# Kernel tuning notes

Hardware: AMD Instinct MI355X
Metric: run time of the kernel (lower is better)

Reference implementation:

```python
import jax, jax.numpy as jnp
import numpy as np
from jax.scipy.linalg import expm

S = 64          # alphabet size (codons)
M = 8           # number of models, prod(model_shape)
N_LEAVES = 32   # leaves of the balanced binary tree
N_EDGES = 62    # nodes 0..62, every non-root node has one parent edge (edge id == child node id)
B = 1024        # batch (alignment columns)
# per-level ranges of child-node ids; node 32+j has children (2j, 2j+1), etc.
LEVELS = [(0, 32), (32, 48), (48, 56), (56, 60), (60, 62)]


def inv_stereographic_projection(p):
    # maps R^{s-1} -> unit sphere S^{s-1}
    n2 = jnp.sum(p * p, axis=-1, keepdims=True)
    return jnp.concatenate([2.0 * p / (n2 + 1.0), (n2 - 1.0) / (n2 + 1.0)], axis=-1)


def generator(R, pi):
    # R: (M, s(s-1)/2) exchangeabilities, pi: (M, s) stationary distribution
    iu, ju = np.triu_indices(S, 1)
    A = jnp.zeros((M, S, S), R.dtype).at[:, iu, ju].set(R).at[:, ju, iu].set(R)
    Q = A * pi[:, None, :]                       # Q_ij = A_ij * pi_j (off-diagonal)
    row = jnp.sum(Q, axis=-1)                    # (M, S)
    return Q - jnp.eye(S, dtype=Q.dtype) * row[:, :, None]


def felsenstein(leave_configuration, R_inv, pi_inv, lengths):
    pi = inv_stereographic_projection(pi_inv) ** 2           # (M, S), rows sum to 1
    R = jnp.exp(R_inv)                                       # positive rates
    Q = generator(R, pi)                                     # (M, S, S)
    tQ = lengths[:, None, None, None] * Q[None]              # (E, M, S, S)
    P = jax.vmap(expm)(tQ.reshape(-1, S, S)).reshape(N_EDGES, M, S, S)
    # leaf alphas: tile leaf observations over the M models -> (n_leaves, B, M, S)
    prev = jnp.broadcast_to(
        leave_configuration.transpose(1, 0, 2)[:, :, None, :],
        (N_LEAVES, leave_configuration.shape[0], M, S))
    # level-synchronous pruning: messages up each parent edge, then product of the two children
    for a, b in LEVELS:
        msg = jnp.einsum('emcd,ebmd->ebmc', P[a:b], prev)    # per-edge transition
        prev = msg[0::2] * msg[1::2]                         # combine sibling pairs
    root = prev[0]                                           # (B, M, S)
    out = jnp.einsum('bms,ms->bm', root, pi)                 # P(data | model m)
    return out.reshape(out.shape[0], M)                      # (B, *model_shape)


def setup_inputs() -> dict:
    key = jax.random.key(0)
    k1, k2, k3, k4 = jax.random.split(key, 4)
    leave_configuration = jax.random.uniform(k1, (B, N_LEAVES, S), dtype=jnp.float32)
    tree_indices = jnp.zeros((B,), dtype=jnp.int32)          # single tree (F=1)
    R_inv = jax.random.uniform(k2, (M, S * (S - 1) // 2), dtype=jnp.float32,
                               minval=-1.0, maxval=1.0)
    pi_inv = jnp.full((M, S - 1), 1.0 / (np.sqrt(S) - 1.0), dtype=jnp.float32) \
        + 0.01 * jax.random.normal(k3, (M, S - 1), dtype=jnp.float32)
    lengths = jax.random.uniform(k4, (N_EDGES,), dtype=jnp.float32,
                                 minval=0.05, maxval=0.5)
    return {'leave_configuration': leave_configuration, 'R_inv': R_inv,
            'pi_inv': pi_inv, 'lengths': lengths, 'tree_indices': tree_indices}


def reference(leave_configuration, R_inv, pi_inv, lengths, tree_indices):
    # F=1: tf.dynamic_partition/gather_nd batch slicing is the identity, so
    # tree_indices is closed over / unused.
    return felsenstein(leave_configuration, R_inv, pi_inv, lengths)
```

## Files before the change

### kernel.cpp

```cpp
#include <hip/hip_runtime.h>

typedef unsigned short u16;
typedef unsigned int u32;
typedef __attribute__((ext_vector_type(8))) __bf16 bf16x8;
typedef __attribute__((ext_vector_type(4))) float f32x4;

constexpr int NS = 64, NM = 8, NB = 1024, SP = 68;

constexpr size_t OFF_QP  = 0;
constexpr size_t OFF_PI  = 393216;
constexpr size_t OFF_PBH = 393728;
constexpr size_t OFF_PBL = OFF_PBH + 1015808;

union FR { uint4 u; bf16x8 v; };
struct Frag { FR h, l; };

__device__ __forceinline__ void split_bf16(float x, u16& h, u16& l) {
  u32 b = __float_as_uint(x);
  u32 hb = (b + 0x7fffu + ((b >> 16) & 1u)) & 0xffff0000u;
  h = (u16)(hb >> 16);
  float r = x - __uint_as_float(hb);
  l = (u16)(__float_as_uint(r) >> 16);
}

__device__ __forceinline__ void mfma3(f32x4& a, const Frag& A, const FR& Bh,
                                      const FR& Bl) {
  a = __builtin_amdgcn_mfma_f32_16x16x32_bf16(A.h.v, Bh.v, a, 0, 0, 0);
  a = __builtin_amdgcn_mfma_f32_16x16x32_bf16(A.h.v, Bl.v, a, 0, 0, 0);
  a = __builtin_amdgcn_mfma_f32_16x16x32_bf16(A.l.v, Bh.v, a, 0, 0, 0);
}

__device__ __forceinline__ void acc4(float* a, const float4 pv,
                                     const float4 q0, const float4 q1,
                                     const float4 q2, const float4 q3) {
  a[0] = fmaf(pv.x, q0.x, fmaf(pv.y, q1.x, fmaf(pv.z, q2.x, fmaf(pv.w, q3.x, a[0]))));
  a[1] = fmaf(pv.x, q0.y, fmaf(pv.y, q1.y, fmaf(pv.z, q2.y, fmaf(pv.w, q3.y, a[1]))));
  a[2] = fmaf(pv.x, q0.z, fmaf(pv.y, q1.z, fmaf(pv.z, q2.z, fmaf(pv.w, q3.z, a[2]))));
  a[3] = fmaf(pv.x, q0.w, fmaf(pv.y, q1.w, fmaf(pv.z, q2.w, fmaf(pv.w, q3.w, a[3]))));
}

__device__ __forceinline__ void mm_tile_store(const float* __restrict__ A,
                                              const float* __restrict__ B,
                                              float* __restrict__ C, int tid) {
  const int c0 = (tid & 15) * 4, r0 = (tid >> 4) * 4;
  float acc[4][4] = {};
  #pragma unroll 4
  for (int k = 0; k < NS; k += 4) {
    const float4 b0 = *(const float4*)&B[(k + 0) * SP + c0];
    const float4 b1 = *(const float4*)&B[(k + 1) * SP + c0];
    const float4 b2 = *(const float4*)&B[(k + 2) * SP + c0];
    const float4 b3 = *(const float4*)&B[(k + 3) * SP + c0];
    #pragma unroll
    for (int r = 0; r < 4; ++r) {
      const float4 av = *(const float4*)&A[(r0 + r) * SP + k];
      acc4(acc[r], av, b0, b1, b2, b3);
    }
  }
  #pragma unroll
  for (int r = 0; r < 4; ++r)
    *(float4*)&C[(r0 + r) * 64 + c0] =
        make_float4(acc[r][0], acc[r][1], acc[r][2], acc[r][3]);
}

__global__ __launch_bounds__(256) void k_setup(const float* __restrict__ R_inv,
                                               const float* __restrict__ pi_inv,
                                               float* __restrict__ ws) {
  const int m = blockIdx.x;
  const int tid = threadIdx.x;
  __shared__ float pis[NS];
  __shared__ float Qs[NS * SP];
  __shared__ float n2s;
  if (tid < 64) {
    float p = (tid < NS - 1) ? pi_inv[m * (NS - 1) + tid] : 0.f;
    float v = p * p;
    #pragma unroll
    for (int off = 32; off; off >>= 1) v += __shfl_down(v, off, 64);
    if (tid == 0) n2s = v;
  }
  __syncthreads();
  const float n2 = n2s;
  if (tid < 64) {
    const float den = n2 + 1.f;
    float x;
    if (tid < NS - 1) { float p = pi_inv[m * (NS - 1) + tid]; x = 2.f * p / den; }
    else              { x = (n2 - 1.f) / den; }
    const float pv = x * x;
    pis[tid] = pv;
    ws[OFF_PI + (size_t)m * NS + tid] = pv;
  }
  __syncthreads();
  for (int idx = tid; idx < NS * NS; idx += 256) {
    const int i = idx >> 6, j = idx & 63;
    float q = 0.f;
    if (i != j) {
      const int a = min(i, j), b = max(i, j);
      const int k = a * (2 * NS - a - 1) / 2 + (b - a - 1);
      q = expf(R_inv[m * (NS * (NS - 1) / 2) + k]) * pis[j];
    }
    Qs[i * SP + j] = q;
  }
  __syncthreads();
  if (tid < 64) {
    float sum = 0.f;
    for (int j = 0; j < NS; ++j) sum += Qs[tid * SP + j];
    Qs[tid * SP + tid] = -sum;
  }
  __syncthreads();
  float* q1 = ws + OFF_QP + (size_t)m * 12 * 4096;
  for (int idx = tid; idx < NS * NS; idx += 256)
    q1[idx] = Qs[(idx >> 6) * SP + (idx & 63)];
  mm_tile_store(Qs, Qs, q1 + 4096, tid);
}

__global__ __launch_bounds__(256) void k_mm(float* __restrict__ ws, int4 t0, int4 t1,
                                            int4 t2, int4 t3) {
  const int m = blockIdx.x, job = blockIdx.y;
  const int4 T = (job == 0) ? t0 : (job == 1) ? t1 : (job == 2) ? t2 : t3;
  const float* A = ws + OFF_QP + ((size_t)m * 12 + (T.y - 1)) * 4096;
  const float* B = ws + OFF_QP + ((size_t)m * 12 + (T.z - 1)) * 4096;
  float* C = ws + OFF_QP + ((size_t)m * 12 + (T.x - 1)) * 4096;
  const int tid = threadIdx.x;
  __shared__ float As[NS * SP], Bs[NS * SP];
  for (int idx = tid; idx < 4096; idx += 256) {
    As[(idx >> 6) * SP + (idx & 63)] = A[idx];
    Bs[(idx >> 6) * SP + (idx & 63)] = B[idx];
  }
  __syncthreads();
  mm_tile_store(As, Bs, C, tid);
}

__global__ __launch_bounds__(256) void k_combine(const float* __restrict__ lengths,
                                                 float* __restrict__ ws) {
  const int e = blockIdx.x, m = blockIdx.y, tid = threadIdx.x;
  const float t = lengths[e];
  const float* qp = ws + OFF_QP + (size_t)m * 12 * 4096;
  u16* ph = (u16*)(ws + OFF_PBH) + (((size_t)e * NM + m) << 12);
  u16* pl = (u16*)(ws + OFF_PBL) + (((size_t)e * NM + m) << 12);
  float acc[16];
  #pragma unroll
  for (int r = 0; r < 16; ++r) {
    const int idx = tid + 256 * r;
    acc[r] = ((idx >> 6) == (idx & 63)) ? 1.f : 0.f;
  }
  float cf = 1.f;
  for (int k = 1; k <= 12; ++k) {
    cf *= t / (float)k;
    const float* qk = qp + (size_t)(k - 1) * 4096;
    #pragma unroll
    for (int r = 0; r < 16; ++r) acc[r] = fmaf(cf, qk[tid + 256 * r], acc[r]);
  }
  #pragma unroll
  for (int r = 0; r < 16; ++r) {
    u16 h, l;
    split_bf16(acc[r], h, l);
    ph[tid + 256 * r] = h;
    pl[tid + 256 * r] = l;
  }
}

__global__ __launch_bounds__(512) void k_tree(
    const float* __restrict__ leaves, const u16* __restrict__ Phi,
    const u16* __restrict__ Plo, const float* __restrict__ ws,
    float* __restrict__ out) {
  const int m = blockIdx.x & 7, btile = blockIdx.x >> 3;
  const int tid = threadIdx.x, lane = tid & 63, w = tid >> 6;
  const int ln = lane & 15, kq = lane >> 4;
  __shared__ u32 nodes[16 * 2048];
  __shared__ float part[2][4][16];

  const f32x4 z = {0.f, 0.f, 0.f, 0.f};

  auto do_pair = [&](int p, int eb, int in_shift, int out_slot, int bt0, int bt1,
                     int ct0, int ct1, bool lvl0, f32x4 (*rootout)[2]) {
    FR Bh[2][2][2], Bl[2][2][2];
    #pragma unroll
    for (int s = 0; s < 2; ++s)
      #pragma unroll
      for (int bt = 0; bt < 2; ++bt) {
        if (bt < bt0 || bt > bt1) continue;
        #pragma unroll
        for (int kh = 0; kh < 2; ++kh) {
          if (lvl0) {
            const int b = btile * 32 + bt * 16 + ln;
            const float* g = leaves + (size_t)b * 2048 + (eb + 2 * p + s) * 64 +
                             kh * 32 + kq * 8;
            const float4 v0 = *(const float4*)g;
            const float4 v1 = *(const float4*)(g + 4);
            u16 h[8], l[8];
            split_bf16(v0.x, h[0], l[0]); split_bf16(v0.y, h[1], l[1]);
            split_bf16(v0.z, h[2], l[2]); split_bf16(v0.w, h[3], l[3]);
            split_bf16(v1.x, h[4], l[4]); split_bf16(v1.y, h[5], l[5]);
            split_bf16(v1.z, h[6], l[6]); split_bf16(v1.w, h[7], l[7]);
            uint4 uh, ul;
            uh.x = h[0] | ((u32)h[1] << 16); uh.y = h[2] | ((u32)h[3] << 16);
            uh.z = h[4] | ((u32)h[5] << 16); uh.w = h[6] | ((u32)h[7] << 16);
            ul.x = l[0] | ((u32)l[1] << 16); ul.y = l[2] | ((u32)l[3] << 16);
            ul.z = l[4] | ((u32)l[5] << 16); ul.w = l[6] | ((u32)l[7] << 16);
            Bh[s][bt][kh].u = uh;
            Bl[s][bt][kh].u = ul;
          } else {
            const int slot = (2 * p + s) << in_shift;
            const int b = bt * 16 + ln;
            const int base = slot * 2048 + b * 32 + (((kh * 4 + kq) + b) & 7) * 4;
            Bh[s][bt][kh].u = *(const uint4*)&nodes[base];
            Bl[s][bt][kh].u = *(const uint4*)&nodes[base + 1024];
          }
        }
      }
    f32x4 acc0[4][2];
    #pragma unroll
    for (int ct = 0; ct < 4; ++ct)
      #pragma unroll
      for (int bt = 0; bt < 2; ++bt) acc0[ct][bt] = z;
    const size_t pb0 = ((size_t)(eb + 2 * p) * NM + m) << 12;
    const size_t pb1 = ((size_t)(eb + 2 * p + 1) * NM + m) << 12;
    #pragma unroll
    for (int ct = 0; ct < 4; ++ct) {
      if (ct < ct0 || ct > ct1) continue;
      Frag A[2];
      #pragma unroll
      for (int kh = 0; kh < 2; ++kh) {
        const size_t off = pb0 + (size_t)(ct * 16 + ln) * 64 + kh * 32 + kq * 8;
        A[kh].h.u = *(const uint4*)(Phi + off);
        A[kh].l.u = *(const uint4*)(Plo + off);
      }
      #pragma unroll
      for (int bt = 0; bt < 2; ++bt) {
        if (bt < bt0 || bt > bt1) continue;
        #pragma unroll
        for (int kh = 0; kh < 2; ++kh)
          mfma3(acc0[ct][bt], A[kh], Bh[0][bt][kh], Bl[0][bt][kh]);
      }
    }
    #pragma unroll
    for (int ct = 0; ct < 4; ++ct) {
      if (ct < ct0 || ct > ct1) continue;
      Frag A[2];
      #pragma unroll
      for (int kh = 0; kh < 2; ++kh) {
        const size_t off = pb1 + (size_t)(ct * 16 + ln) * 64 + kh * 32 + kq * 8;
        A[kh].h.u = *(const uint4*)(Phi + off);
        A[kh].l.u = *(const uint4*)(Plo + off);
      }
      #pragma unroll
      for (int bt = 0; bt < 2; ++bt) {
        if (bt < bt0 || bt > bt1) continue;
        f32x4 a1 = z;
        #pragma unroll
        for (int kh = 0; kh < 2; ++kh)
          mfma3(a1, A[kh], Bh[1][bt][kh], Bl[1][bt][kh]);
        f32x4 pr;
        pr.x = acc0[ct][bt].x * a1.x;
        pr.y = acc0[ct][bt].y * a1.y;
        pr.z = acc0[ct][bt].z * a1.z;
        pr.w = acc0[ct][bt].w * a1.w;
        if (rootout) {
          rootout[ct][bt] = pr;
        } else {
          u16 h[4], l[4];
          split_bf16(pr.x, h[0], l[0]); split_bf16(pr.y, h[1], l[1]);
          split_bf16(pr.z, h[2], l[2]); split_bf16(pr.w, h[3], l[3]);
          const int b = bt * 16 + ln;
          const int jc = ct * 2 + (kq >> 1);
          const int base =
              out_slot * 2048 + b * 32 + ((jc + b) & 7) * 4 + (kq & 1) * 2;
          uint2 wh, wl;
          wh.x = h[0] | ((u32)h[1] << 16); wh.y = h[2] | ((u32)h[3] << 16);
          wl.x = l[0] | ((u32)l[1] << 16); wl.y = l[2] | ((u32)l[3] << 16);
          *(uint2*)&nodes[base] = wh;
          *(uint2*)&nodes[base + 1024] = wl;
        }
      }
    }
  };

  do_pair(w, 0, 0, w, 0, 1, 0, 3, true, nullptr);
  do_pair(w + 8, 0, 0, w + 8, 0, 1, 0, 3, true, nullptr);
  __syncthreads();
  do_pair(w, 32, 0, 2 * w, 0, 1, 0, 3, false, nullptr);
  __syncthreads();
  do_pair(w >> 1, 48, 1, 4 * (w >> 1), w & 1, w & 1, 0, 3, false, nullptr);
  __syncthreads();
  if (w < 4)
    do_pair(w >> 1, 56, 2, 8 * (w >> 1), w & 1, w & 1, 0, 3, false, nullptr);
  __syncthreads();
  f32x4 prod[4][2];
  do_pair(0, 60, 3, 0, w >> 2, w >> 2, w & 3, w & 3, false, prod);
  {
    const int ct = w & 3, bt = w >> 2;
    const float4 piv =
        *(const float4*)&ws[OFF_PI + (size_t)m * 64 + ct * 16 + kq * 4];
    const f32x4 pr = prod[ct][bt];
    float v = pr.x * piv.x + pr.y * piv.y + pr.z * piv.z + pr.w * piv.w;
    v += __shfl_xor(v, 16, 64);
    v += __shfl_xor(v, 32, 64);
    if (lane < 16) part[bt][ct][lane] = v;
  }
  __syncthreads();
  if (tid < 32) {
    const int bt = tid >> 4, bl = tid & 15;
    const float s =
        part[bt][0][bl] + part[bt][1][bl] + part[bt][2][bl] + part[bt][3][bl];
    out[(size_t)(btile * 32 + tid) * 8 + m] = s;
  }
}

extern "C" void kernel_launch(void* const* d_in, const int* in_sizes, int n_in,
                              void* d_out, int out_size, void* d_ws, size_t ws_size,
                              hipStream_t stream) {
  const float* leaves  = (const float*)d_in[0];
  const float* R_inv   = (const float*)d_in[1];
  const float* pi_inv  = (const float*)d_in[2];
  const float* lengths = (const float*)d_in[3];
  float* out = (float*)d_out;
  float* ws  = (float*)d_ws;

  u16* PBH = (u16*)(ws + OFF_PBH);
  u16* PBL = (u16*)(ws + OFF_PBL);

  hipLaunchKernelGGL(k_setup, dim3(NM), dim3(256), 0, stream, R_inv, pi_inv, ws);
  hipLaunchKernelGGL(k_mm, dim3(NM, 2), dim3(256), 0, stream, ws,
                     make_int4(3, 1, 2, 0), make_int4(4, 2, 2, 0),
                     make_int4(4, 2, 2, 0), make_int4(4, 2, 2, 0));
  hipLaunchKernelGGL(k_mm, dim3(NM, 4), dim3(256), 0, stream, ws,
                     make_int4(5, 1, 4, 0), make_int4(6, 2, 4, 0),
                     make_int4(7, 3, 4, 0), make_int4(8, 4, 4, 0));
  hipLaunchKernelGGL(k_mm, dim3(NM, 4), dim3(256), 0, stream, ws,
                     make_int4(9, 1, 8, 0), make_int4(10, 2, 8, 0),
                     make_int4(11, 3, 8, 0), make_int4(12, 4, 8, 0));
  hipLaunchKernelGGL(k_combine, dim3(62, NM), dim3(256), 0, stream, lengths, ws);
  hipLaunchKernelGGL(k_tree, dim3(256), dim3(512), 0, stream, leaves, PBH, PBL,
                     ws, out);
}
```

Before: 139.6 us.

## Fuse P-matrix setup into one MFMA Horner kernel and retile tree kernel

```diff
diff --git a/kernel.cpp b/kernel.cpp
--- a/kernel.cpp
+++ b/kernel.cpp
@@ -5,15 +5,13 @@
 typedef __attribute__((ext_vector_type(8))) __bf16 bf16x8;
 typedef __attribute__((ext_vector_type(4))) float f32x4;
 
-constexpr int NS = 64, NM = 8, NB = 1024, SP = 68;
-
-constexpr size_t OFF_QP  = 0;
-constexpr size_t OFF_PI  = 393216;
-constexpr size_t OFF_PBH = 393728;
+constexpr int NM = 8;
+
+constexpr size_t OFF_PI  = 0;
+constexpr size_t OFF_PBH = 512;
 constexpr size_t OFF_PBL = OFF_PBH + 1015808;
 
 union FR { uint4 u; bf16x8 v; };
-struct Frag { FR h, l; };
 
 __device__ __forceinline__ void split_bf16(float x, u16& h, u16& l) {
   u32 b = __float_as_uint(x);
@@ -23,55 +21,42 @@
   l = (u16)(__float_as_uint(r) >> 16);
 }
 
-__device__ __forceinline__ void mfma3(f32x4& a, const Frag& A, const FR& Bh,
-                                      const FR& Bl) {
-  a = __builtin_amdgcn_mfma_f32_16x16x32_bf16(A.h.v, Bh.v, a, 0, 0, 0);
-  a = __builtin_amdgcn_mfma_f32_16x16x32_bf16(A.h.v, Bl.v, a, 0, 0, 0);
-  a = __builtin_amdgcn_mfma_f32_16x16x32_bf16(A.l.v, Bh.v, a, 0, 0, 0);
-}
-
-__device__ __forceinline__ void acc4(float* a, const float4 pv,
-                                     const float4 q0, const float4 q1,
-                                     const float4 q2, const float4 q3) {
-  a[0] = fmaf(pv.x, q0.x, fmaf(pv.y, q1.x, fmaf(pv.z, q2.x, fmaf(pv.w, q3.x, a[0]))));
-  a[1] = fmaf(pv.x, q0.y, fmaf(pv.y, q1.y, fmaf(pv.z, q2.y, fmaf(pv.w, q3.y, a[1]))));
-  a[2] = fmaf(pv.x, q0.z, fmaf(pv.y, q1.z, fmaf(pv.z, q2.z, fmaf(pv.w, q3.z, a[2]))));
-  a[3] = fmaf(pv.x, q0.w, fmaf(pv.y, q1.w, fmaf(pv.z, q2.w, fmaf(pv.w, q3.w, a[3]))));
-}
-
-__device__ __forceinline__ void mm_tile_store(const float* __restrict__ A,
-                                              const float* __restrict__ B,
-                                              float* __restrict__ C, int tid) {
-  const int c0 = (tid & 15) * 4, r0 = (tid >> 4) * 4;
-  float acc[4][4] = {};
-  #pragma unroll 4
-  for (int k = 0; k < NS; k += 4) {
-    const float4 b0 = *(const float4*)&B[(k + 0) * SP + c0];
-    const float4 b1 = *(const float4*)&B[(k + 1) * SP + c0];
-    const float4 b2 = *(const float4*)&B[(k + 2) * SP + c0];
-    const float4 b3 = *(const float4*)&B[(k + 3) * SP + c0];
-    #pragma unroll
-    for (int r = 0; r < 4; ++r) {
-      const float4 av = *(const float4*)&A[(r0 + r) * SP + k];
-      acc4(acc[r], av, b0, b1, b2, b3);
-    }
-  }
-  #pragma unroll
-  for (int r = 0; r < 4; ++r)
-    *(float4*)&C[(r0 + r) * 64 + c0] =
-        make_float4(acc[r][0], acc[r][1], acc[r][2], acc[r][3]);
-}
-
-__global__ __launch_bounds__(256) void k_setup(const float* __restrict__ R_inv,
-                                               const float* __restrict__ pi_inv,
-                                               float* __restrict__ ws) {
-  const int m = blockIdx.x;
-  const int tid = threadIdx.x;
-  __shared__ float pis[NS];
-  __shared__ float Qs[NS * SP];
+__device__ __forceinline__ void split8(const float4 a, const float4 b,
+                                       uint4& hi, uint4& lo) {
+  u16 h[8], l[8];
+  split_bf16(a.x, h[0], l[0]); split_bf16(a.y, h[1], l[1]);
+  split_bf16(a.z, h[2], l[2]); split_bf16(a.w, h[3], l[3]);
+  split_bf16(b.x, h[4], l[4]); split_bf16(b.y, h[5], l[5]);
+  split_bf16(b.z, h[6], l[6]); split_bf16(b.w, h[7], l[7]);
+  hi.x = h[0] | ((u32)h[1] << 16); hi.y = h[2] | ((u32)h[3] << 16);
+  hi.z = h[4] | ((u32)h[5] << 16); hi.w = h[6] | ((u32)h[7] << 16);
+  lo.x = l[0] | ((u32)l[1] << 16); lo.y = l[2] | ((u32)l[3] << 16);
+  lo.z = l[4] | ((u32)l[5] << 16); lo.w = l[6] | ((u32)l[7] << 16);
+}
+
+__device__ __forceinline__ void mfma3(f32x4& a, const uint4 ah, const uint4 al,
+                                      const uint4 bh, const uint4 bl) {
+  FR Ah, Al, Bh, Bl;
+  Ah.u = ah; Al.u = al; Bh.u = bh; Bl.u = bl;
+  a = __builtin_amdgcn_mfma_f32_16x16x32_bf16(Ah.v, Bh.v, a, 0, 0, 0);
+  a = __builtin_amdgcn_mfma_f32_16x16x32_bf16(Ah.v, Bl.v, a, 0, 0, 0);
+  a = __builtin_amdgcn_mfma_f32_16x16x32_bf16(Al.v, Bh.v, a, 0, 0, 0);
+}
+
+__global__ __launch_bounds__(256, 4) void k_pmats(
+    const float* __restrict__ R_inv, const float* __restrict__ pi_inv,
+    const float* __restrict__ lengths, float* __restrict__ ws,
+    u16* __restrict__ PBH, u16* __restrict__ PBL) {
+  const int e = blockIdx.x, m = blockIdx.y;
+  const int tid = threadIdx.x, lane = tid & 63, w = tid >> 6;
+  const int ln = lane & 15, kq = lane >> 4;
+  __shared__ float pis[64];
   __shared__ float n2s;
+  __shared__ float Qs[64 * 68];
+  __shared__ u32 XT[4096];
+
   if (tid < 64) {
-    float p = (tid < NS - 1) ? pi_inv[m * (NS - 1) + tid] : 0.f;
+    float p = (tid < 63) ? pi_inv[m * 63 + tid] : 0.f;
     float v = p * p;
     #pragma unroll
     for (int off = 32; off; off >>= 1) v += __shfl_down(v, off, 64);
@@ -81,228 +66,211 @@
   const float n2 = n2s;
   if (tid < 64) {
     const float den = n2 + 1.f;
-    float x;
-    if (tid < NS - 1) { float p = pi_inv[m * (NS - 1) + tid]; x = 2.f * p / den; }
-    else              { x = (n2 - 1.f) / den; }
+    const float x = (tid < 63) ? 2.f * pi_inv[m * 63 + tid] / den
+                               : (n2 - 1.f) / den;
     const float pv = x * x;
     pis[tid] = pv;
-    ws[OFF_PI + (size_t)m * NS + tid] = pv;
-  }
-  __syncthreads();
-  for (int idx = tid; idx < NS * NS; idx += 256) {
+    if (e == 0) ws[OFF_PI + (size_t)m * 64 + tid] = pv;
+  }
+  __syncthreads();
+  for (int idx = tid; idx < 4096; idx += 256) {
     const int i = idx >> 6, j = idx & 63;
     float q = 0.f;
     if (i != j) {
       const int a = min(i, j), b = max(i, j);
-      const int k = a * (2 * NS - a - 1) / 2 + (b - a - 1);
-      q = expf(R_inv[m * (NS * (NS - 1) / 2) + k]) * pis[j];
-    }
-    Qs[i * SP + j] = q;
+      const int kk = a * (127 - a) / 2 + (b - a - 1);
+      q = expf(R_inv[m * 2016 + kk]) * pis[j];
+    }
+    Qs[i * 68 + j] = q;
+  }
+  {
+    const int n = tid & 63, cp = (tid >> 6) * 2;
+    #pragma unroll
+    for (int ci = 0; ci < 2; ++ci) {
+      const int c = cp + ci;
+      uint4 hv = {0, 0, 0, 0};
+      const int r = n - 8 * c;
+      if (r >= 0 && r < 8) {
+        const u32 val = (u32)0x3F80u << ((r & 1) * 16);
+        if (r < 2) hv.x = val; else if (r < 4) hv.y = val;
+        else if (r < 6) hv.z = val; else hv.w = val;
+      }
+      const int dw = n * 32 + (((c + n) & 7) << 2);
+      *(uint4*)&XT[dw] = hv;
+      uint4 zz = {0, 0, 0, 0};
+      *(uint4*)&XT[2048 + dw] = zz;
+    }
   }
   __syncthreads();
   if (tid < 64) {
-    float sum = 0.f;
-    for (int j = 0; j < NS; ++j) sum += Qs[tid * SP + j];
-    Qs[tid * SP + tid] = -sum;
-  }
-  __syncthreads();
-  float* q1 = ws + OFF_QP + (size_t)m * 12 * 4096;
-  for (int idx = tid; idx < NS * NS; idx += 256)
-    q1[idx] = Qs[(idx >> 6) * SP + (idx & 63)];
-  mm_tile_store(Qs, Qs, q1 + 4096, tid);
-}
-
-__global__ __launch_bounds__(256) void k_mm(float* __restrict__ ws, int4 t0, int4 t1,
-                                            int4 t2, int4 t3) {
-  const int m = blockIdx.x, job = blockIdx.y;
-  const int4 T = (job == 0) ? t0 : (job == 1) ? t1 : (job == 2) ? t2 : t3;
-  const float* A = ws + OFF_QP + ((size_t)m * 12 + (T.y - 1)) * 4096;
-  const float* B = ws + OFF_QP + ((size_t)m * 12 + (T.z - 1)) * 4096;
-  float* C = ws + OFF_QP + ((size_t)m * 12 + (T.x - 1)) * 4096;
-  const int tid = threadIdx.x;
-  __shared__ float As[NS * SP], Bs[NS * SP];
-  for (int idx = tid; idx < 4096; idx += 256) {
-    As[(idx >> 6) * SP + (idx & 63)] = A[idx];
-    Bs[(idx >> 6) * SP + (idx & 63)] = B[idx];
-  }
-  __syncthreads();
-  mm_tile_store(As, Bs, C, tid);
-}
-
-__global__ __launch_bounds__(256) void k_combine(const float* __restrict__ lengths,
-                                                 float* __restrict__ ws) {
-  const int e = blockIdx.x, m = blockIdx.y, tid = threadIdx.x;
+    float s = 0.f;
+    #pragma unroll 4
+    for (int j4 = 0; j4 < 64; j4 += 4) {
+      const float4 q = *(const float4*)&Qs[tid * 68 + j4];
+      s += q.x + q.y + q.z + q.w;
+    }
+    Qs[tid * 68 + tid] = -s;
+  }
+  __syncthreads();
   const float t = lengths[e];
-  const float* qp = ws + OFF_QP + (size_t)m * 12 * 4096;
-  u16* ph = (u16*)(ws + OFF_PBH) + (((size_t)e * NM + m) << 12);
-  u16* pl = (u16*)(ws + OFF_PBL) + (((size_t)e * NM + m) << 12);
-  float acc[16];
+  uint4 ah[2], al[2];
   #pragma unroll
-  for (int r = 0; r < 16; ++r) {
-    const int idx = tid + 256 * r;
-    acc[r] = ((idx >> 6) == (idx & 63)) ? 1.f : 0.f;
-  }
-  float cf = 1.f;
-  for (int k = 1; k <= 12; ++k) {
-    cf *= t / (float)k;
-    const float* qk = qp + (size_t)(k - 1) * 4096;
+  for (int kh = 0; kh < 2; ++kh) {
+    const float* qr = &Qs[(16 * w + ln) * 68 + kh * 32 + kq * 8];
+    float4 a = *(const float4*)qr, b = *(const float4*)(qr + 4);
+    a.x *= t; a.y *= t; a.z *= t; a.w *= t;
+    b.x *= t; b.y *= t; b.z *= t; b.w *= t;
+    split8(a, b, ah[kh], al[kh]);
+  }
+  const f32x4 z = {0.f, 0.f, 0.f, 0.f};
+  const size_t pb = ((size_t)e * 8 + m) << 12;
+  const int i0 = 16 * w + 4 * kq;
+  for (int k = 12; k >= 1; --k) {
+    __syncthreads();
+    f32x4 acc[4] = {z, z, z, z};
     #pragma unroll
-    for (int r = 0; r < 16; ++r) acc[r] = fmaf(cf, qk[tid + 256 * r], acc[r]);
-  }
-  #pragma unroll
-  for (int r = 0; r < 16; ++r) {
-    u16 h, l;
-    split_bf16(acc[r], h, l);
-    ph[tid + 256 * r] = h;
-    pl[tid + 256 * r] = l;
-  }
-}
-
-__global__ __launch_bounds__(512) void k_tree(
+    for (int bt = 0; bt < 4; ++bt) {
+      const int n = bt * 16 + ln;
+      #pragma unroll
+      for (int kh = 0; kh < 2; ++kh) {
+        const int dw = n * 32 + ((((kh * 4 + kq) + n) & 7) << 2);
+        const uint4 bh = *(const uint4*)&XT[dw];
+        const uint4 bl = *(const uint4*)&XT[2048 + dw];
+        mfma3(acc[bt], ah[kh], al[kh], bh, bl);
+      }
+    }
+    __syncthreads();
+    const float rk = 1.f / (float)k;
+    if (k > 1) {
+      #pragma unroll
+      for (int bt = 0; bt < 4; ++bt) {
+        const int n = bt * 16 + ln;
+        float v[4] = {acc[bt].x * rk, acc[bt].y * rk, acc[bt].z * rk,
+                      acc[bt].w * rk};
+        #pragma unroll
+        for (int r = 0; r < 4; ++r)
+          if (i0 + r == n) v[r] += 1.f;
+        u16 h[4], l[4];
+        split_bf16(v[0], h[0], l[0]); split_bf16(v[1], h[1], l[1]);
+        split_bf16(v[2], h[2], l[2]); split_bf16(v[3], h[3], l[3]);
+        const int dw =
+            n * 32 + ((((2 * w + (kq >> 1)) + n) & 7) << 2) + (kq & 1) * 2;
+        uint2 hh, llv;
+        hh.x = h[0] | ((u32)h[1] << 16); hh.y = h[2] | ((u32)h[3] << 16);
+        llv.x = l[0] | ((u32)l[1] << 16); llv.y = l[2] | ((u32)l[3] << 16);
+        *(uint2*)&XT[dw] = hh;
+        *(uint2*)&XT[2048 + dw] = llv;
+      }
+    } else {
+      #pragma unroll
+      for (int bt = 0; bt < 4; ++bt) {
+        const int n = bt * 16 + ln;
+        float v[4] = {acc[bt].x, acc[bt].y, acc[bt].z, acc[bt].w};
+        #pragma unroll
+        for (int r = 0; r < 4; ++r)
+          if (i0 + r == n) v[r] += 1.f;
+        #pragma unroll
+        for (int r = 0; r < 4; ++r) {
+          u16 h, l;
+          split_bf16(v[r], h, l);
+          const size_t o = pb + (size_t)(i0 + r) * 64 + n;
+          PBH[o] = h;
+          PBL[o] = l;
+        }
+      }
+    }
+  }
+}
+
+__global__ __launch_bounds__(512, 4) void k_tree(
     const float* __restrict__ leaves, const u16* __restrict__ Phi,
     const u16* __restrict__ Plo, const float* __restrict__ ws,
     float* __restrict__ out) {
   const int m = blockIdx.x & 7, btile = blockIdx.x >> 3;
   const int tid = threadIdx.x, lane = tid & 63, w = tid >> 6;
   const int ln = lane & 15, kq = lane >> 4;
-  __shared__ u32 nodes[16 * 2048];
-  __shared__ float part[2][4][16];
-
+  __shared__ float slots[16384];
+  __shared__ float part[4][16];
   const f32x4 z = {0.f, 0.f, 0.f, 0.f};
 
-  auto do_pair = [&](int p, int eb, int in_shift, int out_slot, int bt0, int bt1,
-                     int ct0, int ct1, bool lvl0, f32x4 (*rootout)[2]) {
-    FR Bh[2][2][2], Bl[2][2][2];
-    #pragma unroll
-    for (int s = 0; s < 2; ++s)
-      #pragma unroll
-      for (int bt = 0; bt < 2; ++bt) {
-        if (bt < bt0 || bt > bt1) continue;
+  auto do_pair = [&](int p, int eb, int shift, int out_slot, int ct0, int nct,
+                     bool leaf, f32x4* rootout) {
+    uint4 bh[2], bl[2];
+    f32x4 acc0[4], acc1[4];
+    for (int s = 0; s < 2; ++s) {
+      #pragma unroll
+      for (int kh = 0; kh < 2; ++kh) {
+        float4 xa, xb;
+        if (leaf) {
+          const float* g = leaves + (size_t)(btile * 16 + ln) * 2048 +
+                           (size_t)(eb + 2 * p + s) * 64 + kh * 32 + kq * 8;
+          xa = *(const float4*)g;
+          xb = *(const float4*)(g + 4);
+        } else {
+          const float* nb = slots + ((2 * p + s) << shift) * 1024 + ln * 64;
+          const int cj = kh * 8 + kq * 2;
+          xa = *(const float4*)&nb[((cj + ln) & 15) << 2];
+          xb = *(const float4*)&nb[((cj + 1 + ln) & 15) << 2];
+        }
+        split8(xa, xb, bh[kh], bl[kh]);
+      }
+      const size_t pbase = ((size_t)(eb + 2 * p + s) * 8 + m) << 12;
+      f32x4* acc = s ? acc1 : acc0;
+      #pragma unroll 4
+      for (int ci = 0; ci < nct; ++ci) {
+        const int ct = ct0 + ci;
+        f32x4 a = z;
         #pragma unroll
         for (int kh = 0; kh < 2; ++kh) {
-          if (lvl0) {
-            const int b = btile * 32 + bt * 16 + ln;
-            const float* g = leaves + (size_t)b * 2048 + (eb + 2 * p + s) * 64 +
-                             kh * 32 + kq * 8;
-            const float4 v0 = *(const float4*)g;
-            const float4 v1 = *(const float4*)(g + 4);
-            u16 h[8], l[8];
-            split_bf16(v0.x, h[0], l[0]); split_bf16(v0.y, h[1], l[1]);
-            split_bf16(v0.z, h[2], l[2]); split_bf16(v0.w, h[3], l[3]);
-            split_bf16(v1.x, h[4], l[4]); split_bf16(v1.y, h[5], l[5]);
-            split_bf16(v1.z, h[6], l[6]); split_bf16(v1.w, h[7], l[7]);
-            uint4 uh, ul;
-            uh.x = h[0] | ((u32)h[1] << 16); uh.y = h[2] | ((u32)h[3] << 16);
-            uh.z = h[4] | ((u32)h[5] << 16); uh.w = h[6] | ((u32)h[7] << 16);
-            ul.x = l[0] | ((u32)l[1] << 16); ul.y = l[2] | ((u32)l[3] << 16);
-            ul.z = l[4] | ((u32)l[5] << 16); ul.w = l[6] | ((u32)l[7] << 16);
-            Bh[s][bt][kh].u = uh;
-            Bl[s][bt][kh].u = ul;
-          } else {
-            const int slot = (2 * p + s) << in_shift;
-            const int b = bt * 16 + ln;
-            const int base = slot * 2048 + b * 32 + (((kh * 4 + kq) + b) & 7) * 4;
-            Bh[s][bt][kh].u = *(const uint4*)&nodes[base];
-            Bl[s][bt][kh].u = *(const uint4*)&nodes[base + 1024];
-          }
+          const size_t off = pbase + (size_t)(ct * 16 + ln) * 64 + kh * 32 + kq * 8;
+          const uint4 pah = *(const uint4*)(Phi + off);
+          const uint4 pal = *(const uint4*)(Plo + off);
+          mfma3(a, pah, pal, bh[kh], bl[kh]);
         }
-      }
-    f32x4 acc0[4][2];
-    #pragma unroll
-    for (int ct = 0; ct < 4; ++ct)
-      #pragma unroll
-      for (int bt = 0; bt < 2; ++bt) acc0[ct][bt] = z;
-    const size_t pb0 = ((size_t)(eb + 2 * p) * NM + m) << 12;
-    const size_t pb1 = ((size_t)(eb + 2 * p + 1) * NM + m) << 12;
-    #pragma unroll
-    for (int ct = 0; ct < 4; ++ct) {
-      if (ct < ct0 || ct > ct1) continue;
-      Frag A[2];
-      #pragma unroll
-      for (int kh = 0; kh < 2; ++kh) {
-        const size_t off = pb0 + (size_t)(ct * 16 + ln) * 64 + kh * 32 + kq * 8;
-        A[kh].h.u = *(const uint4*)(Phi + off);
-        A[kh].l.u = *(const uint4*)(Plo + off);
-      }
-      #pragma unroll
-      for (int bt = 0; bt < 2; ++bt) {
-        if (bt < bt0 || bt > bt1) continue;
-        #pragma unroll
-        for (int kh = 0; kh < 2; ++kh)
-          mfma3(acc0[ct][bt], A[kh], Bh[0][bt][kh], Bl[0][bt][kh]);
-      }
-    }
-    #pragma unroll
-    for (int ct = 0; ct < 4; ++ct) {
-      if (ct < ct0 || ct > ct1) continue;
-      Frag A[2];
-      #pragma unroll
-      for (int kh = 0; kh < 2; ++kh) {
-        const size_t off = pb1 + (size_t)(ct * 16 + ln) * 64 + kh * 32 + kq * 8;
-        A[kh].h.u = *(const uint4*)(Phi + off);
-        A[kh].l.u = *(const uint4*)(Plo + off);
-      }
-      #pragma unroll
-      for (int bt = 0; bt < 2; ++bt) {
-        if (bt < bt0 || bt > bt1) continue;
-        f32x4 a1 = z;
-        #pragma unroll
-        for (int kh = 0; kh < 2; ++kh)
-          mfma3(a1, A[kh], Bh[1][bt][kh], Bl[1][bt][kh]);
-        f32x4 pr;
-        pr.x = acc0[ct][bt].x * a1.x;
-        pr.y = acc0[ct][bt].y * a1.y;
-        pr.z = acc0[ct][bt].z * a1.z;
-        pr.w = acc0[ct][bt].w * a1.w;
-        if (rootout) {
-          rootout[ct][bt] = pr;
-        } else {
-          u16 h[4], l[4];
-          split_bf16(pr.x, h[0], l[0]); split_bf16(pr.y, h[1], l[1]);
-          split_bf16(pr.z, h[2], l[2]); split_bf16(pr.w, h[3], l[3]);
-          const int b = bt * 16 + ln;
-          const int jc = ct * 2 + (kq >> 1);
-          const int base =
-              out_slot * 2048 + b * 32 + ((jc + b) & 7) * 4 + (kq & 1) * 2;
-          uint2 wh, wl;
-          wh.x = h[0] | ((u32)h[1] << 16); wh.y = h[2] | ((u32)h[3] << 16);
-          wl.x = l[0] | ((u32)l[1] << 16); wl.y = l[2] | ((u32)l[3] << 16);
-          *(uint2*)&nodes[base] = wh;
-          *(uint2*)&nodes[base + 1024] = wl;
-        }
+        acc[ci] = a;
+      }
+    }
+    #pragma unroll 4
+    for (int ci = 0; ci < nct; ++ci) {
+      f32x4 pr;
+      pr.x = acc0[ci].x * acc1[ci].x;
+      pr.y = acc0[ci].y * acc1[ci].y;
+      pr.z = acc0[ci].z * acc1[ci].z;
+      pr.w = acc0[ci].w * acc1[ci].w;
+      if (rootout) {
+        *rootout = pr;
+      } else {
+        const int ct = ct0 + ci;
+        float* nb = slots + out_slot * 1024 + ln * 64;
+        *(float4*)&nb[(((ct * 4 + kq) + ln) & 15) << 2] =
+            make_float4(pr.x, pr.y, pr.z, pr.w);
       }
     }
   };
 
-  do_pair(w, 0, 0, w, 0, 1, 0, 3, true, nullptr);
-  do_pair(w + 8, 0, 0, w + 8, 0, 1, 0, 3, true, nullptr);
-  __syncthreads();
-  do_pair(w, 32, 0, 2 * w, 0, 1, 0, 3, false, nullptr);
-  __syncthreads();
-  do_pair(w >> 1, 48, 1, 4 * (w >> 1), w & 1, w & 1, 0, 3, false, nullptr);
-  __syncthreads();
-  if (w < 4)
-    do_pair(w >> 1, 56, 2, 8 * (w >> 1), w & 1, w & 1, 0, 3, false, nullptr);
-  __syncthreads();
-  f32x4 prod[4][2];
-  do_pair(0, 60, 3, 0, w >> 2, w >> 2, w & 3, w & 3, false, prod);
-  {
-    const int ct = w & 3, bt = w >> 2;
+  do_pair(w, 0, 0, w, 0, 4, true, nullptr);
+  do_pair(w + 8, 0, 0, w + 8, 0, 4, true, nullptr);
+  __syncthreads();
+  do_pair(w, 32, 0, 2 * w, 0, 4, false, nullptr);
+  __syncthreads();
+  do_pair(w >> 1, 48, 1, 4 * (w >> 1), (w & 1) * 2, 2, false, nullptr);
+  __syncthreads();
+  do_pair(w >> 2, 56, 2, 8 * (w >> 2), w & 3, 1, false, nullptr);
+  __syncthreads();
+  if (w < 4) {
+    f32x4 prod = z;
+    do_pair(0, 60, 3, -1, w, 1, false, &prod);
     const float4 piv =
-        *(const float4*)&ws[OFF_PI + (size_t)m * 64 + ct * 16 + kq * 4];
-    const f32x4 pr = prod[ct][bt];
-    float v = pr.x * piv.x + pr.y * piv.y + pr.z * piv.z + pr.w * piv.w;
+        *(const float4*)&ws[OFF_PI + (size_t)m * 64 + w * 16 + kq * 4];
+    float v = prod.x * piv.x + prod.y * piv.y + prod.z * piv.z + prod.w * piv.w;
     v += __shfl_xor(v, 16, 64);
     v += __shfl_xor(v, 32, 64);
-    if (lane < 16) part[bt][ct][lane] = v;
-  }
-  __syncthreads();
-  if (tid < 32) {
-    const int bt = tid >> 4, bl = tid & 15;
-    const float s =
-        part[bt][0][bl] + part[bt][1][bl] + part[bt][2][bl] + part[bt][3][bl];
-    out[(size_t)(btile * 32 + tid) * 8 + m] = s;
-  }
+    if (lane < 16) part[w][lane] = v;
+  }
+  __syncthreads();
+  if (tid < 16)
+    out[(size_t)(btile * 16 + tid) * 8 + m] =
+        part[0][tid] + part[1][tid] + part[2][tid] + part[3][tid];
 }
 
 extern "C" void kernel_launch(void* const* d_in, const int* in_sizes, int n_in,
@@ -318,17 +286,8 @@
   u16* PBH = (u16*)(ws + OFF_PBH);
   u16* PBL = (u16*)(ws + OFF_PBL);
 
-  hipLaunchKernelGGL(k_setup, dim3(NM), dim3(256), 0, stream, R_inv, pi_inv, ws);
-  hipLaunchKernelGGL(k_mm, dim3(NM, 2), dim3(256), 0, stream, ws,
-                     make_int4(3, 1, 2, 0), make_int4(4, 2, 2, 0),
-                     make_int4(4, 2, 2, 0), make_int4(4, 2, 2, 0));
-  hipLaunchKernelGGL(k_mm, dim3(NM, 4), dim3(256), 0, stream, ws,
-                     make_int4(5, 1, 4, 0), make_int4(6, 2, 4, 0),
-                     make_int4(7, 3, 4, 0), make_int4(8, 4, 4, 0));
-  hipLaunchKernelGGL(k_mm, dim3(NM, 4), dim3(256), 0, stream, ws,
-                     make_int4(9, 1, 8, 0), make_int4(10, 2, 8, 0),
-                     make_int4(11, 3, 8, 0), make_int4(12, 4, 8, 0));
-  hipLaunchKernelGGL(k_combine, dim3(62, NM), dim3(256), 0, stream, lengths, ws);
-  hipLaunchKernelGGL(k_tree, dim3(256), dim3(512), 0, stream, leaves, PBH, PBL,
+  hipLaunchKernelGGL(k_pmats, dim3(62, NM), dim3(256), 0, stream, R_inv, pi_inv,
+                     lengths, ws, PBH, PBL);
+  hipLaunchKernelGGL(k_tree, dim3(512), dim3(512), 0, stream, leaves, PBH, PBL,
                      ws, out);
 }
```

New measurement: 148.3 us. 1.06x slower.
